# Optimization experiments

Hardware: AMD Instinct MI355X
Metric: run time of the kernel (lower is better)

The kernel has to match this reference:

```python
import jax, jax.numpy as jnp
import numpy as np

D_K = 16
TAU = 1.0


def gumbel_softmax_hard(logits, key, tau=TAU):
    # logits: [B, M]; straight-through hard gumbel-softmax along axis 1
    u = jax.random.uniform(key, logits.shape, minval=1e-10, maxval=1.0)
    g = -jnp.log(-jnp.log(u))
    y_soft = jax.nn.softmax((logits + g) / tau, axis=1)
    idx = jnp.argmax(y_soft, axis=1)
    y_hard = jax.nn.one_hot(idx, logits.shape[1], dtype=logits.dtype)
    return jax.lax.stop_gradient(y_hard - y_soft) + y_soft


def setup_inputs() -> dict:
    key = jax.random.key(0)
    k1, k2, k3, k4 = jax.random.split(key, 4)
    B, NR, NW, DR, DW = 32768, 5, 5, 512, 512
    q = jax.random.normal(k1, (B, NR, DR), dtype=jnp.float32)
    k = jax.random.normal(k2, (B, NW, DW), dtype=jnp.float32)
    # GroupLinearLayer weights: [num_blocks, d_in, d_k], init 0.01*randn (NPS convention)
    w_read = 0.01 * jax.random.normal(k3, (NR, DR, D_K), dtype=jnp.float32)
    w_write = 0.01 * jax.random.normal(k4, (NW, DW, D_K), dtype=jnp.float32)
    return {"q": q, "k": k, "w_read": w_read, "w_write": w_write}


def reference(q, k, w_read, w_write):
    temp = jnp.sqrt(jnp.asarray(D_K, dtype=q.dtype))
    # group-linear (block-diagonal) projections
    read = jnp.einsum('bnd,ndk->bnk', q, w_read)    # [B, NR, d_k]
    write = jnp.einsum('bmd,mdk->bmk', k, w_write)  # [B, NW, d_k]
    # scores for the first two read slots against all write slots
    scores_1 = jnp.einsum('bk,bmk->bm', read[:, 0], write) / temp  # [B, NW]
    scores_2 = jnp.einsum('bk,bmk->bm', read[:, 1], write) / temp  # [B, NW]
    g1 = gumbel_softmax_hard(scores_1, jax.random.key(42))
    g2 = gumbel_softmax_hard(scores_2, jax.random.key(43))
    return (g1, g2)
```

## Files before the change

kernel.cpp:

```cpp
#include <hip/hip_runtime.h>
#include <stdint.h>
#include <math.h>

#define NB    32768
#define NSLOT 5
#define DIM   512
#define DK    16

#define RPB    64
#define TPB    512
#define CH     128
#define NCHUNK 4
#define NSL    7
#define NIT    (NSL * NCHUNK)
#define ROWSTRIDE (NSLOT * DIM)

__device__ __forceinline__ uint32_t rotl32(uint32_t x, uint32_t r) {
  return (x << r) | (x >> (32u - r));
}

__device__ __forceinline__ void threefry2x32_20(uint32_t k0, uint32_t k1,
                                                uint32_t& x0, uint32_t& x1) {
  const uint32_t ks[3] = {k0, k1, k0 ^ k1 ^ 0x1BD11BDAu};
  const uint32_t rotA[4] = {13u, 15u, 26u, 6u};
  const uint32_t rotB[4] = {17u, 29u, 16u, 24u};
  x0 += ks[0];
  x1 += ks[1];
#pragma unroll
  for (int i = 0; i < 5; ++i) {
#pragma unroll
    for (int j = 0; j < 4; ++j) {
      uint32_t r = (i & 1) ? rotB[j] : rotA[j];
      x0 += x1;
      x1 = rotl32(x1, r);
      x1 ^= x0;
    }
    x0 += ks[(i + 1) % 3];
    x1 += ks[(i + 2) % 3] + (uint32_t)(i + 1);
  }
}

__device__ __forceinline__ uint32_t jax_random_bits_part(uint32_t key_lo, uint32_t i) {
  uint32_t x0 = 0u;
  uint32_t x1 = i;
  threefry2x32_20(0u, key_lo, x0, x1);
  return x0 ^ x1;
}

__global__ __launch_bounds__(TPB) void csa_kernel(
    const float* __restrict__ q,
    const float* __restrict__ kin,
    const float* __restrict__ wr,
    const float* __restrict__ ww,
    float* __restrict__ out)
{
  __shared__ __align__(16) float buf[2][RPB * CH];

  const int t      = threadIdx.x;
  const int lane   = t & 63;
  const int kg     = __builtin_amdgcn_readfirstlane(t >> 6);
  const int c0     = kg * 2;
  const int r7     = lane & 7;
  const int row_g0 = blockIdx.x * RPB;

  const int t5  = t >> 5;
  const int d4s = t & 31;

  float rcomp[2][2];
  float pscr[10];
  float acc0 = 0.f, acc1 = 0.f;

  auto aslot = [&](int s) -> const float* {
    return (s < 2) ? (q + (size_t)row_g0 * ROWSTRIDE + s * DIM)
                   : (kin + (size_t)row_g0 * ROWSTRIDE + (s - 2) * DIM);
  };

  float4 sreg[4];

  {
    const float* ab = aslot(0);
#pragma unroll
    for (int jj = 0; jj < 4; ++jj) {
      int sr = jj * 16 + t5;
      sreg[jj] = *(const float4*)(ab + (size_t)sr * ROWSTRIDE + d4s * 4);
    }
#pragma unroll
    for (int jj = 0; jj < 4; ++jj) {
      int sr = jj * 16 + t5;
      *(float4*)(&buf[0][sr * CH + ((d4s ^ (sr & 7)) << 2)]) = sreg[jj];
    }
  }
  __syncthreads();

#pragma unroll 1
  for (int it = 0; it < NIT; ++it) {
    const int s   = it >> 2;
    const int c   = it & 3;
    const int nit = it + 1;

    if (nit < NIT) {
      const int ns = nit >> 2, nc = nit & 3;
      const float* ab = aslot(ns) + nc * CH;
#pragma unroll
      for (int jj = 0; jj < 4; ++jj) {
        int sr = jj * 16 + t5;
        sreg[jj] = *(const float4*)(ab + (size_t)sr * ROWSTRIDE + d4s * 4);
      }
    }

    {
      const float* wsl = (s < 2) ? (wr + s * (DIM * DK)) : (ww + (s - 2) * (DIM * DK));
      const float* wp  = wsl + c * (CH * DK) + c0;
      const float* bp  = &buf[it & 1][lane * CH];
#pragma unroll
      for (int d4 = 0; d4 < 32; ++d4) {
        const float4 av = *(const float4*)(bp + ((d4 ^ r7) << 2));
        const float* wd = wp + d4 * 4 * DK;
        float2 w0 = *(const float2*)(wd + 0 * DK);
        float2 w1 = *(const float2*)(wd + 1 * DK);
        float2 w2 = *(const float2*)(wd + 2 * DK);
        float2 w3 = *(const float2*)(wd + 3 * DK);
        acc0 = fmaf(av.x, w0.x, acc0); acc1 = fmaf(av.x, w0.y, acc1);
        acc0 = fmaf(av.y, w1.x, acc0); acc1 = fmaf(av.y, w1.y, acc1);
        acc0 = fmaf(av.z, w2.x, acc0); acc1 = fmaf(av.z, w2.y, acc1);
        acc0 = fmaf(av.w, w3.x, acc0); acc1 = fmaf(av.w, w3.y, acc1);
      }
    }

    if (c == 3) {
      if (s < 2) {
        rcomp[s][0] = acc0; rcomp[s][1] = acc1;
      } else {
        const int m = s - 2;
        pscr[0 * NSLOT + m] = rcomp[0][0] * acc0 + rcomp[0][1] * acc1;
        pscr[1 * NSLOT + m] = rcomp[1][0] * acc0 + rcomp[1][1] * acc1;
      }
      acc0 = 0.f; acc1 = 0.f;
    }

    if (nit < NIT) {
      float* bd = &buf[nit & 1][0];
#pragma unroll
      for (int jj = 0; jj < 4; ++jj) {
        int sr = jj * 16 + t5;
        *(float4*)(bd + sr * CH + ((d4s ^ (sr & 7)) << 2)) = sreg[jj];
      }
    }
    __syncthreads();
  }

  float* psc = &buf[0][0];
  {
    float* pd = psc + (kg * RPB + lane) * 10;
#pragma unroll
    for (int j = 0; j < 10; ++j) pd[j] = pscr[j];
  }
  __syncthreads();

  if (t < RPB) {
    const int row_g = row_g0 + t;
    float sc[10];
#pragma unroll
    for (int j = 0; j < 10; ++j) {
      float sum = 0.f;
#pragma unroll
      for (int g = 0; g < 8; ++g) sum += psc[(g * RPB + t) * 10 + j];
      sc[j] = sum * 0.25f;
    }
#pragma unroll
    for (int n = 0; n < 2; ++n) {
      const uint32_t key_lo = (n == 0) ? 42u : 43u;
      int best = 0;
      float bestv = -INFINITY;
#pragma unroll
      for (int m = 0; m < NSLOT; ++m) {
        uint32_t i = (uint32_t)(row_g * NSLOT + m);
        uint32_t bits = jax_random_bits_part(key_lo, i);
        float f = __uint_as_float((bits >> 9) | 0x3F800000u) - 1.0f;
        float u = fmaxf(1e-10f, f + 1e-10f);
        double tt = -log((double)u);
        float gmb = (float)(-log(tt));
        float z = sc[n * NSLOT + m] + gmb;
        if (z > bestv) { bestv = z; best = m; }
      }
      float* o = out + (size_t)n * (NB * NSLOT) + (size_t)row_g * NSLOT;
#pragma unroll
      for (int m = 0; m < NSLOT; ++m) o[m] = (m == best) ? 1.0f : 0.0f;
    }
  }
}

extern "C" void kernel_launch(void* const* d_in, const int* in_sizes, int n_in,
                              void* d_out, int out_size, void* d_ws, size_t ws_size,
                              hipStream_t stream) {
  const float* q  = (const float*)d_in[0];
  const float* k  = (const float*)d_in[1];
  const float* wr = (const float*)d_in[2];
  const float* ww = (const float*)d_in[3];
  float* out = (float*)d_out;

  dim3 grid(NB / RPB);
  dim3 block(TPB);
  csa_kernel<<<grid, block, 0, stream>>>(q, k, wr, ww, out);
}
```

Measured before the change: 906.9 us.

## Stage activation chunks with direct global-to-LDS loads and unroll slot loop

```diff
diff --git a/kernel.cpp b/kernel.cpp
--- a/kernel.cpp
+++ b/kernel.cpp
@@ -10,9 +10,7 @@
 #define RPB    64
 #define TPB    512
 #define CH     128
-#define NCHUNK 4
 #define NSL    7
-#define NIT    (NSL * NCHUNK)
 #define ROWSTRIDE (NSLOT * DIM)
 
 __device__ __forceinline__ uint32_t rotl32(uint32_t x, uint32_t r) {
@@ -47,7 +45,22 @@
   return x0 ^ x1;
 }
 
-__global__ __launch_bounds__(TPB) void csa_kernel(
+__device__ __forceinline__ void gload_lds16(const float* g, float* l) {
+  __builtin_amdgcn_global_load_lds(
+      (const __attribute__((address_space(1))) void*)g,
+      (__attribute__((address_space(3))) void*)l, 16, 0, 0);
+}
+
+__device__ __forceinline__ void stage_chunk(const float* src, size_t goff,
+                                            float* dst, int kg) {
+#pragma unroll
+  for (int jj = 0; jj < 4; ++jj) {
+    gload_lds16(src + goff + (size_t)jj * (16 * ROWSTRIDE),
+                dst + jj * 2048 + kg * 256);
+  }
+}
+
+__global__ __launch_bounds__(TPB, 2) void csa_kernel(
     const float* __restrict__ q,
     const float* __restrict__ kin,
     const float* __restrict__ wr,
@@ -62,91 +75,64 @@
   const int c0     = kg * 2;
   const int r7     = lane & 7;
   const int row_g0 = blockIdx.x * RPB;
+  const size_t base = (size_t)row_g0 * ROWSTRIDE;
 
-  const int t5  = t >> 5;
-  const int d4s = t & 31;
+  const int t5    = t >> 5;
+  const int d4src = (t & 31) ^ (t5 & 7);
+  const size_t goff = (size_t)t5 * ROWSTRIDE + (size_t)(d4src * 4);
 
   float rcomp[2][2];
   float pscr[10];
   float acc0 = 0.f, acc1 = 0.f;
 
-  auto aslot = [&](int s) -> const float* {
-    return (s < 2) ? (q + (size_t)row_g0 * ROWSTRIDE + s * DIM)
-                   : (kin + (size_t)row_g0 * ROWSTRIDE + (s - 2) * DIM);
-  };
-
-  float4 sreg[4];
-
-  {
-    const float* ab = aslot(0);
-#pragma unroll
-    for (int jj = 0; jj < 4; ++jj) {
-      int sr = jj * 16 + t5;
-      sreg[jj] = *(const float4*)(ab + (size_t)sr * ROWSTRIDE + d4s * 4);
-    }
-#pragma unroll
-    for (int jj = 0; jj < 4; ++jj) {
-      int sr = jj * 16 + t5;
-      *(float4*)(&buf[0][sr * CH + ((d4s ^ (sr & 7)) << 2)]) = sreg[jj];
-    }
-  }
+  stage_chunk(q + base, goff, &buf[0][0], kg);
   __syncthreads();
 
+#pragma unroll
+  for (int s = 0; s < NSL; ++s) {
+    const float* asrc  = (s < 2) ? (q + base + (size_t)s * DIM)
+                                 : (kin + base + (size_t)(s - 2) * DIM);
+    const float* wslot = (s < 2) ? (wr + s * (DIM * DK))
+                                 : (ww + (s - 2) * (DIM * DK));
 #pragma unroll 1
-  for (int it = 0; it < NIT; ++it) {
-    const int s   = it >> 2;
-    const int c   = it & 3;
-    const int nit = it + 1;
+    for (int c = 0; c < 4; ++c) {
+      if (c < 3) {
+        stage_chunk(asrc + (size_t)(c + 1) * CH, goff,
+                    &buf[(c + 1) & 1][0], kg);
+      } else if (s < NSL - 1) {
+        const float* nsrc = (s + 1 < 2) ? (q + base + (size_t)(s + 1) * DIM)
+                                        : (kin + base + (size_t)(s - 1) * DIM);
+        stage_chunk(nsrc, goff, &buf[(c + 1) & 1][0], kg);
+      }
 
-    if (nit < NIT) {
-      const int ns = nit >> 2, nc = nit & 3;
-      const float* ab = aslot(ns) + nc * CH;
+      {
+        const float* bp = &buf[c & 1][lane * CH];
+        const float* wp = wslot + c * (CH * DK) + c0;
 #pragma unroll
-      for (int jj = 0; jj < 4; ++jj) {
-        int sr = jj * 16 + t5;
-        sreg[jj] = *(const float4*)(ab + (size_t)sr * ROWSTRIDE + d4s * 4);
+        for (int d4 = 0; d4 < 32; ++d4) {
+          const float4 av = *(const float4*)(bp + ((d4 ^ r7) << 2));
+          const float* wd = wp + d4 * (4 * DK);
+          float2 w0 = *(const float2*)(wd + 0 * DK);
+          float2 w1 = *(const float2*)(wd + 1 * DK);
+          float2 w2 = *(const float2*)(wd + 2 * DK);
+          float2 w3 = *(const float2*)(wd + 3 * DK);
+          acc0 = fmaf(av.x, w0.x, acc0); acc1 = fmaf(av.x, w0.y, acc1);
+          acc0 = fmaf(av.y, w1.x, acc0); acc1 = fmaf(av.y, w1.y, acc1);
+          acc0 = fmaf(av.z, w2.x, acc0); acc1 = fmaf(av.z, w2.y, acc1);
+          acc0 = fmaf(av.w, w3.x, acc0); acc1 = fmaf(av.w, w3.y, acc1);
+        }
       }
+      __syncthreads();
     }
 
-    {
-      const float* wsl = (s < 2) ? (wr + s * (DIM * DK)) : (ww + (s - 2) * (DIM * DK));
-      const float* wp  = wsl + c * (CH * DK) + c0;
-      const float* bp  = &buf[it & 1][lane * CH];
-#pragma unroll
-      for (int d4 = 0; d4 < 32; ++d4) {
-        const float4 av = *(const float4*)(bp + ((d4 ^ r7) << 2));
-        const float* wd = wp + d4 * 4 * DK;
-        float2 w0 = *(const float2*)(wd + 0 * DK);
-        float2 w1 = *(const float2*)(wd + 1 * DK);
-        float2 w2 = *(const float2*)(wd + 2 * DK);
-        float2 w3 = *(const float2*)(wd + 3 * DK);
-        acc0 = fmaf(av.x, w0.x, acc0); acc1 = fmaf(av.x, w0.y, acc1);
-        acc0 = fmaf(av.y, w1.x, acc0); acc1 = fmaf(av.y, w1.y, acc1);
-        acc0 = fmaf(av.z, w2.x, acc0); acc1 = fmaf(av.z, w2.y, acc1);
-        acc0 = fmaf(av.w, w3.x, acc0); acc1 = fmaf(av.w, w3.y, acc1);
-      }
+    if (s == 0)      { rcomp[0][0] = acc0; rcomp[0][1] = acc1; }
+    else if (s == 1) { rcomp[1][0] = acc0; rcomp[1][1] = acc1; }
+    else {
+      const int m = s - 2;
+      pscr[0 * NSLOT + m] = rcomp[0][0] * acc0 + rcomp[0][1] * acc1;
+      pscr[1 * NSLOT + m] = rcomp[1][0] * acc0 + rcomp[1][1] * acc1;
     }
-
-    if (c == 3) {
-      if (s < 2) {
-        rcomp[s][0] = acc0; rcomp[s][1] = acc1;
-      } else {
-        const int m = s - 2;
-        pscr[0 * NSLOT + m] = rcomp[0][0] * acc0 + rcomp[0][1] * acc1;
-        pscr[1 * NSLOT + m] = rcomp[1][0] * acc0 + rcomp[1][1] * acc1;
-      }
-      acc0 = 0.f; acc1 = 0.f;
-    }
-
-    if (nit < NIT) {
-      float* bd = &buf[nit & 1][0];
-#pragma unroll
-      for (int jj = 0; jj < 4; ++jj) {
-        int sr = jj * 16 + t5;
-        *(float4*)(bd + sr * CH + ((d4s ^ (sr & 7)) << 2)) = sreg[jj];
-      }
-    }
-    __syncthreads();
+    acc0 = 0.f; acc1 = 0.f;
   }
 
   float* psc = &buf[0][0];
```

Result: faster. 844.4 us (-6.9%).
